# Kernel tuning notes

Measured on AMD Instinct MI355X. Metric: run time of the kernel, lower is better.

The kernel has to match this reference:

```python
import jax, jax.numpy as jnp
import numpy as np
import math

B, S, D, H = 8, 1024, 768, 12
DEPTH = D // H


def setup_inputs() -> dict:
    key = jax.random.key(0)
    ks = jax.random.split(key, 12)
    s = 1.0 / math.sqrt(D)
    return {
        "v": jax.random.normal(ks[0], (B, S, D), jnp.float32),
        "k": jax.random.normal(ks[1], (B, S, D), jnp.float32),
        "q": jax.random.normal(ks[2], (B, S, D), jnp.float32),
        "mask": jnp.zeros((B, 1, 1, S), jnp.float32),
        "adjoin_matrix": jax.random.normal(ks[3], (B, 1, S, S), jnp.float32),
        "wq": jax.random.normal(ks[4], (D, D), jnp.float32) * s,
        "bq": jnp.zeros((D,), jnp.float32),
        "wk": jax.random.normal(ks[5], (D, D), jnp.float32) * s,
        "bk": jnp.zeros((D,), jnp.float32),
        "wv": jax.random.normal(ks[6], (D, D), jnp.float32) * s,
        "bv": jnp.zeros((D,), jnp.float32),
        "wo": jax.random.normal(ks[7], (D, D), jnp.float32) * s,
        "bo": jnp.zeros((D,), jnp.float32),
    }


def _split_heads(x):  # (B,S,D) -> (B,H,S,depth)
    return x.reshape(B, S, H, DEPTH).transpose(0, 2, 1, 3)


def reference(v, k, q, mask, adjoin_matrix, wq, bq, wk, bk, wv, bv, wo, bo):
    qh = _split_heads(q @ wq + bq)
    kh = _split_heads(k @ wk + bk)
    vh = _split_heads(v @ wv + bv)
    # scores: (B,H,Sq,Sk)
    logits = jnp.einsum("bhqd,bhkd->bhqk", qh, kh) / math.sqrt(DEPTH)
    logits = logits + mask * (-1e9) + adjoin_matrix
    attn = jax.nn.softmax(logits, axis=-1)
    out = jnp.einsum("bhqk,bhkd->bhqd", attn, vh)
    concat = out.transpose(0, 2, 1, 3).reshape(B, S, D)
    output = concat @ wo + bo
    return output, attn
```

## Files before the change

kernel.cpp:

```cpp
#include <hip/hip_runtime.h>
#include <math.h>

#define BB 8
#define SS 1024
#define DD 768
#define HH 12
#define DEP 64

typedef __attribute__((ext_vector_type(8))) short short8;
typedef __attribute__((ext_vector_type(4))) float floatx4;

static __device__ __forceinline__ unsigned short f2bf(float x) {
    union { float f; unsigned u; } v; v.f = x;
    unsigned r = v.u + 0x7fffu + ((v.u >> 16) & 1u);
    return (unsigned short)(r >> 16);
}

__device__ __forceinline__ void gld16(const unsigned short* g, unsigned short* l) {
    __builtin_amdgcn_global_load_lds(
        (const __attribute__((address_space(1))) unsigned int*)g,
        (__attribute__((address_space(3))) unsigned int*)l,
        16, 0, 0);
}

__global__ __launch_bounds__(256) void conv_inputs_kernel(
    const float* __restrict__ q, const float* __restrict__ k,
    const float* __restrict__ v,
    unsigned short* __restrict__ qb, unsigned short* __restrict__ kb,
    unsigned short* __restrict__ vb)
{
    const int y = blockIdx.y;
    const float* src = (y == 0) ? q : (y == 1) ? k : v;
    unsigned short* dst = (y == 0) ? qb : (y == 1) ? kb : vb;
    const size_t i = ((size_t)blockIdx.x * 256 + threadIdx.x) * 4;
    const float4 f = *(const float4*)(src + i);
    ushort4 o;
    o.x = f2bf(f.x); o.y = f2bf(f.y); o.z = f2bf(f.z); o.w = f2bf(f.w);
    *(ushort4*)(dst + i) = o;
}

__global__ __launch_bounds__(256) void conv_wT_kernel(
    const float* __restrict__ wq, const float* __restrict__ wk,
    const float* __restrict__ wv, const float* __restrict__ wo,
    unsigned short* __restrict__ wqT, unsigned short* __restrict__ wkT,
    unsigned short* __restrict__ wvT, unsigned short* __restrict__ woT)
{
    const int z = blockIdx.z;
    const float* W = (z == 0) ? wq : (z == 1) ? wk : (z == 2) ? wv : wo;
    unsigned short* WT = (z == 0) ? wqT : (z == 1) ? wkT : (z == 2) ? wvT : woT;
    __shared__ float tile[32][33];
    const int tx = threadIdx.x & 31, ty = threadIdx.x >> 5;
    const int k0 = blockIdx.y * 32, n0 = blockIdx.x * 32;
#pragma unroll
    for (int r = 0; r < 4; ++r)
        tile[ty + r * 8][tx] = W[(size_t)(k0 + ty + r * 8) * DD + n0 + tx];
    __syncthreads();
#pragma unroll
    for (int r = 0; r < 4; ++r)
        WT[(size_t)(n0 + ty + r * 8) * DD + k0 + tx] = f2bf(tile[tx][ty + r * 8]);
}

__global__ __launch_bounds__(256) void transpose_v_kernel(
    const unsigned short* __restrict__ vh, unsigned short* __restrict__ vhT)
{
    const int t = blockIdx.x, bh = blockIdx.y;
    const unsigned short* src = vh + ((size_t)bh * SS + (size_t)t * 64) * DEP;
    unsigned short* dst = vhT + (size_t)bh * DEP * SS + (size_t)t * 64;
    __shared__ unsigned short tile[64][72];
    const int tid = threadIdx.x;
#pragma unroll
    for (int it = 0; it < 2; ++it) {
        const int f = it * 256 + tid;
        const int row = f >> 3, c8 = (f & 7) * 8;
        *(float4*)&tile[row][c8] = *(const float4*)&src[(size_t)row * DEP + c8];
    }
    __syncthreads();
#pragma unroll
    for (int it = 0; it < 2; ++it) {
        const int f = it * 256 + tid;
        const int drow = f >> 3, s8 = (f & 7) * 8;
        short8 o;
#pragma unroll
        for (int j = 0; j < 8; ++j) o[j] = (short)tile[s8 + j][drow];
        *(short8*)&dst[(size_t)drow * SS + s8] = o;
    }
}

__global__ __launch_bounds__(256) void qkv_gemm_kernel(
    const unsigned short* __restrict__ qb, const unsigned short* __restrict__ kb,
    const unsigned short* __restrict__ vb,
    const unsigned short* __restrict__ wqT, const unsigned short* __restrict__ wkT,
    const unsigned short* __restrict__ wvT,
    const float* __restrict__ bq, const float* __restrict__ bk,
    const float* __restrict__ bv,
    unsigned short* __restrict__ qh, unsigned short* __restrict__ kh,
    unsigned short* __restrict__ vh)
{
    const int z = blockIdx.z;
    const unsigned short* A  = (z == 0) ? qb  : (z == 1) ? kb  : vb;
    const unsigned short* BT = (z == 0) ? wqT : (z == 1) ? wkT : wvT;
    const float* bias        = (z == 0) ? bq  : (z == 1) ? bk  : bv;
    unsigned short* Y        = (z == 0) ? qh  : (z == 1) ? kh  : vh;

    const int m0 = blockIdx.y * 128, n0 = blockIdx.x * 128;
    const int tid = threadIdx.x;
    const int wave = tid >> 6, lane = tid & 63;
    const int quad = lane >> 4, l16 = lane & 15;
    const int wm = (wave & 1) * 64, wn = (wave >> 1) * 64;

    __shared__ unsigned short aS[128][64];
    __shared__ unsigned short bS[128][64];

    const int sr = lane >> 3;
    const int sc = (lane & 7) * 8;

    floatx4 acc[4][4];
#pragma unroll
    for (int i = 0; i < 4; ++i)
#pragma unroll
        for (int j = 0; j < 4; ++j) acc[i][j] = (floatx4){0.f, 0.f, 0.f, 0.f};

    for (int k0 = 0; k0 < DD; k0 += 64) {
        __syncthreads();
#pragma unroll
        for (int i = 0; i < 4; ++i) {
            const int bi = wave * 4 + i;
            const int r = bi * 8 + sr;
            gld16(&A[(size_t)(m0 + r) * DD + k0 + sc], &aS[bi * 8][0]);
            gld16(&BT[(size_t)(n0 + r) * DD + k0 + sc], &bS[bi * 8][0]);
        }
        __syncthreads();
        short8 a[2][4], b[2][4];
#pragma unroll
        for (int kc = 0; kc < 2; ++kc)
#pragma unroll
            for (int t = 0; t < 4; ++t) {
                a[kc][t] = *(const short8*)&aS[wm + t * 16 + l16][kc * 32 + quad * 8];
                b[kc][t] = *(const short8*)&bS[wn + t * 16 + l16][kc * 32 + quad * 8];
            }
#pragma unroll
        for (int kc = 0; kc < 2; ++kc)
#pragma unroll
            for (int tm = 0; tm < 4; ++tm)
#pragma unroll
                for (int tn = 0; tn < 4; ++tn)
                    acc[tm][tn] = __builtin_amdgcn_mfma_f32_16x16x32_bf16(
                        a[kc][tm], b[kc][tn], acc[tm][tn], 0, 0, 0);
    }

#pragma unroll
    for (int tm = 0; tm < 4; ++tm)
#pragma unroll
        for (int tn = 0; tn < 4; ++tn)
#pragma unroll
            for (int r = 0; r < 4; ++r) {
                const int row = m0 + wm + tm * 16 + quad * 4 + r;
                const int col = n0 + wn + tn * 16 + l16;
                const float val = acc[tm][tn][r] + bias[col];
                const int bi = row >> 10, s = row & 1023;
                const int hh = col >> 6, dp = col & 63;
                Y[(((size_t)bi * HH + hh) * SS + s) * DEP + dp] = f2bf(val);
            }
}

__global__ __launch_bounds__(256) void out_gemm_kernel(
    const unsigned short* __restrict__ A, const unsigned short* __restrict__ BT,
    const float* __restrict__ bias, float* __restrict__ Y)
{
    const int m0 = blockIdx.y * 128, n0 = blockIdx.x * 128;
    const int tid = threadIdx.x;
    const int wave = tid >> 6, lane = tid & 63;
    const int quad = lane >> 4, l16 = lane & 15;
    const int wm = (wave & 1) * 64, wn = (wave >> 1) * 64;

    __shared__ unsigned short aS[128][64];
    __shared__ unsigned short bS[128][64];

    const int sr = lane >> 3;
    const int sc = (lane & 7) * 8;

    floatx4 acc[4][4];
#pragma unroll
    for (int i = 0; i < 4; ++i)
#pragma unroll
        for (int j = 0; j < 4; ++j) acc[i][j] = (floatx4){0.f, 0.f, 0.f, 0.f};

    for (int k0 = 0; k0 < DD; k0 += 64) {
        __syncthreads();
#pragma unroll
        for (int i = 0; i < 4; ++i) {
            const int bi = wave * 4 + i;
            const int r = bi * 8 + sr;
            gld16(&A[(size_t)(m0 + r) * DD + k0 + sc], &aS[bi * 8][0]);
            gld16(&BT[(size_t)(n0 + r) * DD + k0 + sc], &bS[bi * 8][0]);
        }
        __syncthreads();
        short8 a[2][4], b[2][4];
#pragma unroll
        for (int kc = 0; kc < 2; ++kc)
#pragma unroll
            for (int t = 0; t < 4; ++t) {
                a[kc][t] = *(const short8*)&aS[wm + t * 16 + l16][kc * 32 + quad * 8];
                b[kc][t] = *(const short8*)&bS[wn + t * 16 + l16][kc * 32 + quad * 8];
            }
#pragma unroll
        for (int kc = 0; kc < 2; ++kc)
#pragma unroll
            for (int tm = 0; tm < 4; ++tm)
#pragma unroll
                for (int tn = 0; tn < 4; ++tn)
                    acc[tm][tn] = __builtin_amdgcn_mfma_f32_16x16x32_bf16(
                        a[kc][tm], b[kc][tn], acc[tm][tn], 0, 0, 0);
    }

#pragma unroll
    for (int tm = 0; tm < 4; ++tm)
#pragma unroll
        for (int tn = 0; tn < 4; ++tn)
#pragma unroll
            for (int r = 0; r < 4; ++r) {
                const int row = m0 + wm + tm * 16 + quad * 4 + r;
                const int col = n0 + wn + tn * 16 + l16;
                Y[(size_t)row * DD + col] = acc[tm][tn][r] + bias[col];
            }
}

__global__ __launch_bounds__(256) void attn_kernel(
    const unsigned short* __restrict__ qh, const unsigned short* __restrict__ kh,
    const unsigned short* __restrict__ vhT, const float* __restrict__ mask,
    const float* __restrict__ adjoin, float* __restrict__ attn_out,
    unsigned short* __restrict__ concat)
{
    const int bid = (blockIdx.x & 7) * 192 + (blockIdx.x >> 3);
    const int rb = bid & 15;
    const int h  = (bid >> 4) % HH;
    const int b  = bid / (16 * HH);
    const int r0 = rb * 64;

    const unsigned short* qbp = qh + ((size_t)(b * HH + h)) * SS * DEP;
    const unsigned short* kbp = kh + ((size_t)(b * HH + h)) * SS * DEP;
    const unsigned short* vTp = vhT + ((size_t)(b * HH + h)) * DEP * SS;
    const float* adj = adjoin + (size_t)b * SS * SS;
    const float* mk  = mask + (size_t)b * SS;
    float* attn = attn_out + ((size_t)(b * HH + h)) * SS * SS;

    __shared__ unsigned short kS[64][72];
    __shared__ unsigned short vS[64][72];
    __shared__ unsigned short qpS[64][72];
    __shared__ float adjS[64][68];
    __shared__ float mS[SS];

    const int tid = threadIdx.x;
    const int wave = tid >> 6, lane = tid & 63;
    const int quad = lane >> 4, l16 = lane & 15;

#pragma unroll
    for (int it = 0; it < 2; ++it) {
        const int f = it * 256 + tid;
        const int row = f >> 3, c8 = (f & 7) * 8;
        *(float4*)&qpS[row][c8] = *(const float4*)&qbp[(size_t)(r0 + row) * DEP + c8];
    }
    *(float4*)&mS[tid * 4] = *(const float4*)&mk[tid * 4];
    __syncthreads();
    const short8 aq0 = *(const short8*)&qpS[wave * 16 + l16][quad * 8];
    const short8 aq1 = *(const short8*)&qpS[wave * 16 + l16][32 + quad * 8];

    float m_[4], l_[4];
#pragma unroll
    for (int r = 0; r < 4; ++r) { m_[r] = -INFINITY; l_[r] = 0.f; }

    for (int t = 0; t < 16; ++t) {
        __syncthreads();
#pragma unroll
        for (int it = 0; it < 2; ++it) {
            const int f = it * 256 + tid;
            const int row = f >> 3, c8 = (f & 7) * 8;
            *(float4*)&kS[row][c8] = *(const float4*)&kbp[(size_t)(t * 64 + row) * DEP + c8];
        }
#pragma unroll
        for (int it = 0; it < 4; ++it) {
            const int row = it * 16 + (tid >> 4), c4 = (tid & 15) * 4;
            *(float4*)&adjS[row][c4] = *(const float4*)&adj[(size_t)(r0 + row) * SS + t * 64 + c4];
        }
        __syncthreads();

        floatx4 sc[4];
        __builtin_amdgcn_s_setprio(1);
#pragma unroll
        for (int tn = 0; tn < 4; ++tn) {
            const short8 b0 = *(const short8*)&kS[tn * 16 + l16][quad * 8];
            const short8 b1 = *(const short8*)&kS[tn * 16 + l16][32 + quad * 8];
            floatx4 z = (floatx4){0.f, 0.f, 0.f, 0.f};
            z = __builtin_amdgcn_mfma_f32_16x16x32_bf16(aq0, b0, z, 0, 0, 0);
            z = __builtin_amdgcn_mfma_f32_16x16x32_bf16(aq1, b1, z, 0, 0, 0);
            sc[tn] = z;
        }
        __builtin_amdgcn_s_setprio(0);

        float lg[4][4];
#pragma unroll
        for (int tn = 0; tn < 4; ++tn) {
            const int cl = tn * 16 + l16;
            const float mv = -1e9f * mS[t * 64 + cl];
#pragma unroll
            for (int r = 0; r < 4; ++r) {
                const int lr = wave * 16 + quad * 4 + r;
                lg[tn][r] = sc[tn][r] * 0.125f + mv + adjS[lr][cl];
            }
        }
#pragma unroll
        for (int r = 0; r < 4; ++r) {
            float tmax = fmaxf(fmaxf(lg[0][r], lg[1][r]), fmaxf(lg[2][r], lg[3][r]));
            tmax = fmaxf(tmax, __shfl_xor(tmax, 1));
            tmax = fmaxf(tmax, __shfl_xor(tmax, 2));
            tmax = fmaxf(tmax, __shfl_xor(tmax, 4));
            tmax = fmaxf(tmax, __shfl_xor(tmax, 8));
            const float mn = fmaxf(m_[r], tmax);
            float ps = __expf(lg[0][r] - mn) + __expf(lg[1][r] - mn)
                     + __expf(lg[2][r] - mn) + __expf(lg[3][r] - mn);
            ps += __shfl_xor(ps, 1);
            ps += __shfl_xor(ps, 2);
            ps += __shfl_xor(ps, 4);
            ps += __shfl_xor(ps, 8);
            l_[r] = l_[r] * __expf(m_[r] - mn) + ps;
            m_[r] = mn;
        }
    }

    float invl[4];
#pragma unroll
    for (int r = 0; r < 4; ++r) invl[r] = 1.0f / l_[r];

    floatx4 oacc[4];
#pragma unroll
    for (int tn = 0; tn < 4; ++tn) oacc[tn] = (floatx4){0.f, 0.f, 0.f, 0.f};

    for (int t = 0; t < 16; ++t) {
        __syncthreads();
#pragma unroll
        for (int it = 0; it < 2; ++it) {
            const int f = it * 256 + tid;
            const int row = f >> 3, c8 = (f & 7) * 8;
            *(float4*)&kS[row][c8] = *(const float4*)&kbp[(size_t)(t * 64 + row) * DEP + c8];
            *(float4*)&vS[row][c8] = *(const float4*)&vTp[(size_t)row * SS + t * 64 + c8];
        }
#pragma unroll
        for (int it = 0; it < 4; ++it) {
            const int row = it * 16 + (tid >> 4), c4 = (tid & 15) * 4;
            *(float4*)&adjS[row][c4] = *(const float4*)&adj[(size_t)(r0 + row) * SS + t * 64 + c4];
        }
        __syncthreads();

        floatx4 sc[4];
        __builtin_amdgcn_s_setprio(1);
#pragma unroll
        for (int tn = 0; tn < 4; ++tn) {
            const short8 b0 = *(const short8*)&kS[tn * 16 + l16][quad * 8];
            const short8 b1 = *(const short8*)&kS[tn * 16 + l16][32 + quad * 8];
            floatx4 z = (floatx4){0.f, 0.f, 0.f, 0.f};
            z = __builtin_amdgcn_mfma_f32_16x16x32_bf16(aq0, b0, z, 0, 0, 0);
            z = __builtin_amdgcn_mfma_f32_16x16x32_bf16(aq1, b1, z, 0, 0, 0);
            sc[tn] = z;
        }
        __builtin_amdgcn_s_setprio(0);

#pragma unroll
        for (int tn = 0; tn < 4; ++tn) {
            const int cl = tn * 16 + l16;
            const float mv = -1e9f * mS[t * 64 + cl];
#pragma unroll
            for (int r = 0; r < 4; ++r) {
                const int lr = wave * 16 + quad * 4 + r;
                const float lgv = sc[tn][r] * 0.125f + mv + adjS[lr][cl];
                const float p = __expf(lgv - m_[r]) * invl[r];
                adjS[lr][cl] = p;
                qpS[lr][cl] = f2bf(p);
            }
        }
        __syncthreads();

        const short8 ap0 = *(const short8*)&qpS[wave * 16 + l16][quad * 8];
        const short8 ap1 = *(const short8*)&qpS[wave * 16 + l16][32 + quad * 8];
        __builtin_amdgcn_s_setprio(1);
#pragma unroll
        for (int tn = 0; tn < 4; ++tn) {
            const short8 bv0 = *(const short8*)&vS[tn * 16 + l16][quad * 8];
            const short8 bv1 = *(const short8*)&vS[tn * 16 + l16][32 + quad * 8];
            oacc[tn] = __builtin_amdgcn_mfma_f32_16x16x32_bf16(ap0, bv0, oacc[tn], 0, 0, 0);
            oacc[tn] = __builtin_amdgcn_mfma_f32_16x16x32_bf16(ap1, bv1, oacc[tn], 0, 0, 0);
        }
        __builtin_amdgcn_s_setprio(0);

#pragma unroll
        for (int it = 0; it < 4; ++it) {
            const int row = it * 16 + (tid >> 4), c4 = (tid & 15) * 4;
            const float4 pv = *(const float4*)&adjS[row][c4];
            *(float4*)&attn[(size_t)(r0 + row) * SS + t * 64 + c4] = pv;
        }
    }

#pragma unroll
    for (int tn = 0; tn < 4; ++tn)
#pragma unroll
        for (int r = 0; r < 4; ++r) {
            const int s = r0 + wave * 16 + quad * 4 + r;
            const int dp = tn * 16 + l16;
            concat[((size_t)b * SS + s) * DD + h * DEP + dp] = f2bf(oacc[tn][r]);
        }
}

extern "C" void kernel_launch(void* const* d_in, const int* in_sizes, int n_in,
                              void* d_out, int out_size, void* d_ws, size_t ws_size,
                              hipStream_t stream)
{
    (void)in_sizes; (void)n_in; (void)out_size; (void)ws_size;

    const float* v      = (const float*)d_in[0];
    const float* k      = (const float*)d_in[1];
    const float* q      = (const float*)d_in[2];
    const float* mask   = (const float*)d_in[3];
    const float* adjoin = (const float*)d_in[4];
    const float* wq     = (const float*)d_in[5];
    const float* bq     = (const float*)d_in[6];
    const float* wk     = (const float*)d_in[7];
    const float* bk     = (const float*)d_in[8];
    const float* wv     = (const float*)d_in[9];
    const float* bv     = (const float*)d_in[10];
    const float* wo     = (const float*)d_in[11];
    const float* bo     = (const float*)d_in[12];

    float* out  = (float*)d_out;
    float* attn = out + (size_t)BB * SS * DD;

    const size_t N1 = (size_t)BB * SS * DD;
    const size_t NW = (size_t)DD * DD;
    unsigned short* ws = (unsigned short*)d_ws;
    unsigned short* qb      = ws;
    unsigned short* kb      = ws + N1;
    unsigned short* vb      = ws + 2 * N1;
    unsigned short* qhb     = ws + 3 * N1;
    unsigned short* khb     = ws + 4 * N1;
    unsigned short* vhb     = ws + 5 * N1;
    unsigned short* concatb = ws + 6 * N1;
    unsigned short* wqT     = ws + 7 * N1;
    unsigned short* wkT     = wqT + NW;
    unsigned short* wvT     = wkT + NW;
    unsigned short* woT     = wvT + NW;
    unsigned short* vhT     = qb;

    conv_inputs_kernel<<<dim3((unsigned)(N1 / 4 / 256), 3), 256, 0, stream>>>(
        q, k, v, qb, kb, vb);
    conv_wT_kernel<<<dim3(24, 24, 4), 256, 0, stream>>>(
        wq, wk, wv, wo, wqT, wkT, wvT, woT);

    qkv_gemm_kernel<<<dim3(DD / 128, (BB * SS) / 128, 3), 256, 0, stream>>>(
        qb, kb, vb, wqT, wkT, wvT, bq, bk, bv, qhb, khb, vhb);

    transpose_v_kernel<<<dim3(SS / 64, BB * HH), 256, 0, stream>>>(vhb, vhT);

    attn_kernel<<<dim3(16 * HH * BB), 256, 0, stream>>>(
        qhb, khb, vhT, mask, adjoin, attn, concatb);

    out_gemm_kernel<<<dim3(DD / 128, (BB * SS) / 128), 256, 0, stream>>>(
        concatb, woT, bo, out);
}
```

Baseline: 730.6 us.

## Double-buffer GEMM LDS tiles and drop attention block barrier via wave-local stores

The QKV and output projection GEMMs now keep two LDS buffers and prefetch the next K tile while MFMAs run on the current one. This leaves one barrier per iteration instead of two, and MFMA sections are wrapped in s_setprio. In the attention kernel, each wave now writes back only its own 16 rows of probabilities, so the block-wide __syncthreads before the PV MFMA is removed. The cost is doubled LDS use in the GEMMs, which may reduce occupancy. Dropping the barrier also depends on qpS and adjS rows being touched only by their own wave.

```diff
diff --git a/kernel.cpp b/kernel.cpp
--- a/kernel.cpp
+++ b/kernel.cpp
@@ -108,8 +108,8 @@
     const int quad = lane >> 4, l16 = lane & 15;
     const int wm = (wave & 1) * 64, wn = (wave >> 1) * 64;
 
-    __shared__ unsigned short aS[128][64];
-    __shared__ unsigned short bS[128][64];
+    __shared__ unsigned short aS[2][128][64];
+    __shared__ unsigned short bS[2][128][64];
 
     const int sr = lane >> 3;
     const int sc = (lane & 7) * 8;
@@ -120,24 +120,37 @@
 #pragma unroll
         for (int j = 0; j < 4; ++j) acc[i][j] = (floatx4){0.f, 0.f, 0.f, 0.f};
 
-    for (int k0 = 0; k0 < DD; k0 += 64) {
-        __syncthreads();
-#pragma unroll
-        for (int i = 0; i < 4; ++i) {
-            const int bi = wave * 4 + i;
-            const int r = bi * 8 + sr;
-            gld16(&A[(size_t)(m0 + r) * DD + k0 + sc], &aS[bi * 8][0]);
-            gld16(&BT[(size_t)(n0 + r) * DD + k0 + sc], &bS[bi * 8][0]);
-        }
-        __syncthreads();
+#pragma unroll
+    for (int i = 0; i < 4; ++i) {
+        const int bi = wave * 4 + i;
+        const int r = bi * 8 + sr;
+        gld16(&A[(size_t)(m0 + r) * DD + sc], &aS[0][bi * 8][0]);
+        gld16(&BT[(size_t)(n0 + r) * DD + sc], &bS[0][bi * 8][0]);
+    }
+    __syncthreads();
+
+#pragma unroll
+    for (int t = 0; t < 12; ++t) {
+        const int cur = t & 1;
+        if (t < 11) {
+            const int k1 = (t + 1) * 64;
+#pragma unroll
+            for (int i = 0; i < 4; ++i) {
+                const int bi = wave * 4 + i;
+                const int r = bi * 8 + sr;
+                gld16(&A[(size_t)(m0 + r) * DD + k1 + sc], &aS[cur ^ 1][bi * 8][0]);
+                gld16(&BT[(size_t)(n0 + r) * DD + k1 + sc], &bS[cur ^ 1][bi * 8][0]);
+            }
+        }
         short8 a[2][4], b[2][4];
 #pragma unroll
         for (int kc = 0; kc < 2; ++kc)
 #pragma unroll
-            for (int t = 0; t < 4; ++t) {
-                a[kc][t] = *(const short8*)&aS[wm + t * 16 + l16][kc * 32 + quad * 8];
-                b[kc][t] = *(const short8*)&bS[wn + t * 16 + l16][kc * 32 + quad * 8];
-            }
+            for (int tt = 0; tt < 4; ++tt) {
+                a[kc][tt] = *(const short8*)&aS[cur][wm + tt * 16 + l16][kc * 32 + quad * 8];
+                b[kc][tt] = *(const short8*)&bS[cur][wn + tt * 16 + l16][kc * 32 + quad * 8];
+            }
+        __builtin_amdgcn_s_setprio(1);
 #pragma unroll
         for (int kc = 0; kc < 2; ++kc)
 #pragma unroll
@@ -146,6 +159,8 @@
                 for (int tn = 0; tn < 4; ++tn)
                     acc[tm][tn] = __builtin_amdgcn_mfma_f32_16x16x32_bf16(
                         a[kc][tm], b[kc][tn], acc[tm][tn], 0, 0, 0);
+        __builtin_amdgcn_s_setprio(0);
+        __syncthreads();
     }
 
 #pragma unroll
@@ -173,8 +188,8 @@
     const int quad = lane >> 4, l16 = lane & 15;
     const int wm = (wave & 1) * 64, wn = (wave >> 1) * 64;
 
-    __shared__ unsigned short aS[128][64];
-    __shared__ unsigned short bS[128][64];
+    __shared__ unsigned short aS[2][128][64];
+    __shared__ unsigned short bS[2][128][64];
 
     const int sr = lane >> 3;
     const int sc = (lane & 7) * 8;
@@ -185,24 +200,37 @@
 #pragma unroll
         for (int j = 0; j < 4; ++j) acc[i][j] = (floatx4){0.f, 0.f, 0.f, 0.f};
 
-    for (int k0 = 0; k0 < DD; k0 += 64) {
-        __syncthreads();
-#pragma unroll
-        for (int i = 0; i < 4; ++i) {
-            const int bi = wave * 4 + i;
-            const int r = bi * 8 + sr;
-            gld16(&A[(size_t)(m0 + r) * DD + k0 + sc], &aS[bi * 8][0]);
-            gld16(&BT[(size_t)(n0 + r) * DD + k0 + sc], &bS[bi * 8][0]);
-        }
-        __syncthreads();
+#pragma unroll
+    for (int i = 0; i < 4; ++i) {
+        const int bi = wave * 4 + i;
+        const int r = bi * 8 + sr;
+        gld16(&A[(size_t)(m0 + r) * DD + sc], &aS[0][bi * 8][0]);
+        gld16(&BT[(size_t)(n0 + r) * DD + sc], &bS[0][bi * 8][0]);
+    }
+    __syncthreads();
+
+#pragma unroll
+    for (int t = 0; t < 12; ++t) {
+        const int cur = t & 1;
+        if (t < 11) {
+            const int k1 = (t + 1) * 64;
+#pragma unroll
+            for (int i = 0; i < 4; ++i) {
+                const int bi = wave * 4 + i;
+                const int r = bi * 8 + sr;
+                gld16(&A[(size_t)(m0 + r) * DD + k1 + sc], &aS[cur ^ 1][bi * 8][0]);
+                gld16(&BT[(size_t)(n0 + r) * DD + k1 + sc], &bS[cur ^ 1][bi * 8][0]);
+            }
+        }
         short8 a[2][4], b[2][4];
 #pragma unroll
         for (int kc = 0; kc < 2; ++kc)
 #pragma unroll
-            for (int t = 0; t < 4; ++t) {
-                a[kc][t] = *(const short8*)&aS[wm + t * 16 + l16][kc * 32 + quad * 8];
-                b[kc][t] = *(const short8*)&bS[wn + t * 16 + l16][kc * 32 + quad * 8];
-            }
+            for (int tt = 0; tt < 4; ++tt) {
+                a[kc][tt] = *(const short8*)&aS[cur][wm + tt * 16 + l16][kc * 32 + quad * 8];
+                b[kc][tt] = *(const short8*)&bS[cur][wn + tt * 16 + l16][kc * 32 + quad * 8];
+            }
+        __builtin_amdgcn_s_setprio(1);
 #pragma unroll
         for (int kc = 0; kc < 2; ++kc)
 #pragma unroll
@@ -211,6 +239,8 @@
                 for (int tn = 0; tn < 4; ++tn)
                     acc[tm][tn] = __builtin_amdgcn_mfma_f32_16x16x32_bf16(
                         a[kc][tm], b[kc][tn], acc[tm][tn], 0, 0, 0);
+        __builtin_amdgcn_s_setprio(0);
+        __syncthreads();
     }
 
 #pragma unroll
@@ -377,7 +407,6 @@
                 qpS[lr][cl] = f2bf(p);
             }
         }
-        __syncthreads();
 
         const short8 ap0 = *(const short8*)&qpS[wave * 16 + l16][quad * 8];
         const short8 ap1 = *(const short8*)&qpS[wave * 16 + l16][32 + quad * 8];
@@ -391,11 +420,14 @@
         }
         __builtin_amdgcn_s_setprio(0);
 
-#pragma unroll
-        for (int it = 0; it < 4; ++it) {
-            const int row = it * 16 + (tid >> 4), c4 = (tid & 15) * 4;
-            const float4 pv = *(const float4*)&adjS[row][c4];
-            *(float4*)&attn[(size_t)(r0 + row) * SS + t * 64 + c4] = pv;
+        {
+            const int srow = wave * 16 + (lane >> 2);
+            const int sc0 = (lane & 3) * 4;
+#pragma unroll
+            for (int j = 0; j < 4; ++j) {
+                *(float4*)&attn[(size_t)(r0 + srow) * SS + t * 64 + sc0 + j * 16] =
+                    *(const float4*)&adjS[srow][sc0 + j * 16];
+            }
         }
     }
 
```

Measured after the change: 727.9 us. No clear change (-0.4%).
